# Performance work log

Measured on AMD Instinct MI355X. Metric: run time of the kernel, lower is better.

## Reference

```python
import jax, jax.numpy as jnp
import numpy as np


def setup_inputs() -> dict:
    key = jax.random.key(0)
    ks = jax.random.split(key, 7)
    B, T, I, H = 64, 512, 128, 1024
    s_ih = 1.0 / np.sqrt(H)
    return {
        "x": jax.random.normal(ks[0], (B, T, I), dtype=jnp.float32),
        "W_ih": jax.random.normal(ks[1], (4 * H, I), dtype=jnp.float32) * s_ih,
        "W_hh": jax.random.normal(ks[2], (4 * H, H), dtype=jnp.float32) * s_ih,
        "b_ih": jax.random.normal(ks[3], (4 * H,), dtype=jnp.float32) * s_ih,
        "b_hh": jax.random.normal(ks[4], (4 * H,), dtype=jnp.float32) * s_ih,
        "fc_w": jax.random.normal(ks[5], (I, H), dtype=jnp.float32) * s_ih,
        "fc_b": jax.random.normal(ks[6], (I,), dtype=jnp.float32) * s_ih,
    }


def _lstm_scan(x, W_ih, W_hh, b_ih, b_hh):
    # x: [B, T, I]; returns h sequence [B, T, H]
    B, T, I = x.shape
    H = W_hh.shape[1]
    # precompute input contributions for all timesteps: [T, B, 4H]
    x_proj = jnp.einsum('bti,gi->tbg', x, W_ih) + (b_ih + b_hh)

    def step(carry, xp):
        h, c = carry
        gates = xp + h @ W_hh.T  # [B, 4H]
        i_g, f_g, g_g, o_g = jnp.split(gates, 4, axis=-1)  # PyTorch order i,f,g,o
        i_g = jax.nn.sigmoid(i_g)
        f_g = jax.nn.sigmoid(f_g)
        g_g = jnp.tanh(g_g)
        o_g = jax.nn.sigmoid(o_g)
        c = f_g * c + i_g * g_g
        h = o_g * jnp.tanh(c)
        return (h, c), h

    h0 = jnp.zeros((B, H), dtype=x.dtype)
    c0 = jnp.zeros((B, H), dtype=x.dtype)
    _, hs = jax.lax.scan(step, (h0, c0), x_proj)  # hs: [T, B, H]
    return jnp.transpose(hs, (1, 0, 2))  # [B, T, H]


def reference(x, W_ih, W_hh, b_ih, b_hh, fc_w, fc_b):
    hs = _lstm_scan(x, W_ih, W_hh, b_ih, b_hh)  # [B, T, H]
    return hs @ fc_w.T + fc_b  # [B, T, I]
```

## Files before the change

kernel.cpp:

```cpp
#include <hip/hip_runtime.h>

#define Tn 512
#define Bn 64
#define In 128
#define Hn 1024
#define GBn 16
#define NGn 4
#define NBLKn 32
#define NCOLn 32
#define ROW64 (Hn / 4)

typedef __attribute__((ext_vector_type(8))) short short8;
typedef __attribute__((ext_vector_type(4))) float f32x4;
typedef unsigned long long u64;
typedef unsigned int u32;

__device__ __forceinline__ short f2bf(float f) {
  u32 u = __builtin_bit_cast(u32, f);
  u32 r = u + 0x7FFFu + ((u >> 16) & 1u);
  return (short)(r >> 16);
}
__device__ __forceinline__ float sigm(float x) { return 1.f / (1.f + __expf(-x)); }
__device__ __forceinline__ float tanh_f(float x) {
  float ax = fabsf(x);
  float e = __expf(-2.f * ax);
  float t = (1.f - e) / (1.f + e);
  return x < 0.f ? -t : t;
}
__device__ __forceinline__ short8 cvt8(const float* p) {
  float4 a0 = *(const float4*)p;
  float4 a1 = *(const float4*)(p + 4);
  short8 w;
  w[0] = f2bf(a0.x); w[1] = f2bf(a0.y); w[2] = f2bf(a0.z); w[3] = f2bf(a0.w);
  w[4] = f2bf(a1.x); w[5] = f2bf(a1.y); w[6] = f2bf(a1.z); w[7] = f2bf(a1.w);
  return w;
}

__global__ void __launch_bounds__(256) cvt_kernel(const float* __restrict__ x,
                                                  unsigned short* __restrict__ xb) {
  size_t idx = ((size_t)blockIdx.x * 256 + threadIdx.x) * 8;
  *(short8*)(xb + idx) = cvt8(x + idx);
}

__global__ void __launch_bounds__(512, 2) lstm_kernel(
    const unsigned short* __restrict__ xb, const float* __restrict__ W_ih,
    const float* __restrict__ W_hh, const float* __restrict__ b_ih,
    const float* __restrict__ b_hh, unsigned short* __restrict__ hsb,
    u64* __restrict__ pp) {
  const int bid = blockIdx.x;
  const int grp = bid >> 5;
  const int hc = bid & 31;
  const int tid = threadIdx.x;
  const int wid = tid >> 6;
  const int lane = tid & 63;
  const int rowsel = lane & 15;
  const int k8 = (lane >> 4) * 8;
  const int gate = wid >> 1;
  const int ct = wid & 1;

  __shared__ unsigned short h_lds[GBn * Hn];
  __shared__ float gates_s[4][16][34];
  __shared__ float bias_s[4][NCOLn];

  if (tid < 128) {
    int gg = tid >> 5, cc = tid & 31;
    int idx = gg * Hn + hc * NCOLn + cc;
    bias_s[gg][cc] = b_ih[idx] + b_hh[idx];
  }

  const int wrow = gate * Hn + hc * NCOLn + ct * 16 + rowsel;
  short8 whh[32];
#pragma unroll
  for (int kt = 0; kt < 32; ++kt)
    whh[kt] = cvt8(W_hh + (size_t)wrow * Hn + kt * 32 + k8);
  short8 wih[4];
#pragma unroll
  for (int kt = 0; kt < 4; ++kt)
    wih[kt] = cvt8(W_ih + (size_t)wrow * In + kt * 32 + k8);
  __syncthreads();

  u64* ppg = pp + (size_t)grp * 2 * (GBn * ROW64);
  const unsigned short* xrow = xb + (size_t)(grp * GBn + rowsel) * (Tn * In);

  const int prow = tid >> 5;
  const int pcol = tid & 31;
  float c_reg = 0.f;

  const int rswz = (rowsel & 7) << 4;
  const int rbase = rowsel * 2048 + k8 * 2;

#pragma clang loop unroll(disable)
  for (int t = 0; t < Tn; ++t) {
    f32x4 acc[4];
#pragma unroll
    for (int q = 0; q < 4; ++q) acc[q] = (f32x4){0.f, 0.f, 0.f, 0.f};

    {
      const unsigned short* xp = xrow + (size_t)t * In + k8;
#pragma unroll
      for (int kt = 0; kt < 4; ++kt) {
        short8 a = *(const short8*)(xp + kt * 32);
        acc[kt] = __builtin_amdgcn_mfma_f32_16x16x32_bf16(a, wih[kt], acc[kt],
                                                          0, 0, 0);
      }
    }

    if (t > 0) {
      const u32 want = (u32)((t - 1) % 255) + 1;
      const u64* src64 = ppg + ((t - 1) & 1) * (GBn * ROW64);
      u64 v[8];
      while (true) {
        bool okv = true;
#pragma unroll
        for (int j = 0; j < 8; ++j) {
          const u64* pl =
              src64 + (2 * wid + (j >> 2)) * ROW64 + (j & 3) * 64 + lane;
          v[j] = __hip_atomic_load(pl, __ATOMIC_RELAXED,
                                   __HIP_MEMORY_SCOPE_AGENT);
        }
#pragma unroll
        for (int j = 0; j < 8; ++j)
          okv = okv && ((u32)(v[j] >> 56) == want);
        if (__all(okv)) break;
        __builtin_amdgcn_s_sleep(1);
      }
#pragma unroll
      for (int j = 0; j < 8; ++j) {
        u32 lo = (u32)v[j], hi = (u32)(v[j] >> 32);
        float f0 = (float)(((int)(lo << 20)) >> 20) * 4.8828125e-4f;
        float f1 = (float)(((int)(lo << 8)) >> 20) * 4.8828125e-4f;
        float f2 = (float)(((int)(hi << 20)) >> 20) * 4.8828125e-4f;
        float f3 = (float)(((int)(hi << 8)) >> 20) * 4.8828125e-4f;
        u32 w01, w23;
        asm("v_cvt_pk_bf16_f32 %0, %1, %2" : "=v"(w01) : "v"(f0), "v"(f1));
        asm("v_cvt_pk_bf16_f32 %0, %1, %2" : "=v"(w23) : "v"(f2), "v"(f3));
        int row = 2 * wid + (j >> 2);
        int byteoff = (row * 2048 + ((j & 3) * 64 + lane) * 8) ^
                      ((row & 7) << 4);
        *(u64*)((char*)h_lds + byteoff) = ((u64)w23 << 32) | (u64)w01;
      }
      __syncthreads();

#pragma unroll
      for (int kt = 0; kt < 32; ++kt) {
        short8 a = *(const short8*)((char*)h_lds + ((rbase + kt * 64) ^ rswz));
        acc[kt & 3] = __builtin_amdgcn_mfma_f32_16x16x32_bf16(a, whh[kt],
                                                              acc[kt & 3], 0, 0, 0);
      }
    }

    f32x4 asum = (acc[0] + acc[1]) + (acc[2] + acc[3]);
#pragma unroll
    for (int r = 0; r < 4; ++r)
      gates_s[gate][(lane >> 4) * 4 + r][ct * 16 + (lane & 15)] = asum[r];
    __syncthreads();

    float iv = gates_s[0][prow][pcol] + bias_s[0][pcol];
    float fv = gates_s[1][prow][pcol] + bias_s[1][pcol];
    float gv = gates_s[2][prow][pcol] + bias_s[2][pcol];
    float ov = gates_s[3][prow][pcol] + bias_s[3][pcol];
    float ig = sigm(iv), fg = sigm(fv), og = sigm(ov), gt = tanh_f(gv);
    c_reg = fg * c_reg + ig * gt;
    float hval = og * tanh_f(c_reg);

    int q12 = (int)rintf(hval * 2048.f);
    q12 = q12 > 2047 ? 2047 : (q12 < -2048 ? -2048 : q12);
    u32 me = (u32)(q12 & 0xFFF) << (12 * (pcol & 1));
    u32 m2 = me | __shfl_xor(me, 1);
    u32 mo = __shfl_xor(m2, 2);
    u32 tag = (u32)(t % 255) + 1;
    if ((pcol & 3) == 0) {
      u64 wv = ((u64)(mo | (tag << 24)) << 32) | (u64)m2;
      __hip_atomic_store(
          ppg + (t & 1) * (GBn * ROW64) + prow * ROW64 + (hc * NCOLn + pcol) / 4,
          wv, __ATOMIC_RELAXED, __HIP_MEMORY_SCOPE_AGENT);
    }
    u32 hb = (u32)(unsigned short)f2bf(hval);
    u32 other = __shfl_xor(hb, 1);
    if (!(tid & 1)) {
      size_t hsidx =
          ((size_t)t * Bn + grp * GBn + prow) * Hn + hc * NCOLn + pcol;
      *(u32*)(hsb + hsidx) = hb | (other << 16);
    }
  }
}

__global__ void __launch_bounds__(256) fc_mfma_kernel(
    const unsigned short* __restrict__ hsb, const unsigned short* __restrict__ fwb,
    const float* __restrict__ fcb, float* __restrict__ out) {
  const int wid = threadIdx.x >> 6;
  const int lane = threadIdx.x & 63;
  const int rowsel = lane & 15;
  const int k8 = (lane >> 4) * 8;
  const int r0 = blockIdx.x * 16;
  const int i0 = wid * 32;
  f32x4 acc0 = {0.f, 0.f, 0.f, 0.f}, acc1 = {0.f, 0.f, 0.f, 0.f};
  const unsigned short* hrow = hsb + (size_t)(r0 + rowsel) * Hn + k8;
  const unsigned short* w0 = fwb + (size_t)(i0 + rowsel) * Hn + k8;
  const unsigned short* w1 = w0 + 16 * Hn;
#pragma unroll 8
  for (int kt = 0; kt < 32; ++kt) {
    short8 a = *(const short8*)(hrow + kt * 32);
    short8 b0 = *(const short8*)(w0 + kt * 32);
    short8 b1 = *(const short8*)(w1 + kt * 32);
    acc0 = __builtin_amdgcn_mfma_f32_16x16x32_bf16(a, b0, acc0, 0, 0, 0);
    acc1 = __builtin_amdgcn_mfma_f32_16x16x32_bf16(a, b1, acc1, 0, 0, 0);
  }
  const int n = lane & 15;
  float bias0 = fcb[i0 + n], bias1 = fcb[i0 + 16 + n];
#pragma unroll
  for (int r = 0; r < 4; ++r) {
    int row = r0 + (lane >> 4) * 4 + r;
    float* op = out + ((size_t)(row & 63) * Tn + (row >> 6)) * In;
    op[i0 + n] = acc0[r] + bias0;
    op[i0 + 16 + n] = acc1[r] + bias1;
  }
}

extern "C" void kernel_launch(void* const* d_in, const int* in_sizes, int n_in,
                              void* d_out, int out_size, void* d_ws,
                              size_t ws_size, hipStream_t stream) {
  const float* x    = (const float*)d_in[0];
  const float* W_ih = (const float*)d_in[1];
  const float* W_hh = (const float*)d_in[2];
  const float* b_ih = (const float*)d_in[3];
  const float* b_hh = (const float*)d_in[4];
  const float* fc_w = (const float*)d_in[5];
  const float* fc_b = (const float*)d_in[6];
  float* out = (float*)d_out;

  const size_t hs_b = (size_t)Tn * Bn * Hn * 2;
  const size_t x_b  = (size_t)Bn * Tn * In * 2;
  const size_t fw_b = (size_t)In * Hn * 2;
  const size_t pp_b = (size_t)NGn * 2 * GBn * ROW64 * 8;

  char* wsc = (char*)d_ws;
  unsigned short* hsb = (unsigned short*)wsc;
  unsigned short* xb  = (unsigned short*)(wsc + hs_b);
  unsigned short* fwb = (unsigned short*)(wsc + hs_b + x_b);
  u64* pp = (u64*)(wsc + hs_b + x_b + fw_b);

  (void)hipMemsetAsync(pp, 0, pp_b, stream);
  hipLaunchKernelGGL(cvt_kernel, dim3((Bn * Tn * In) / (256 * 8)), dim3(256),
                     0, stream, x, xb);
  hipLaunchKernelGGL(cvt_kernel, dim3((In * Hn) / (256 * 8)), dim3(256), 0,
                     stream, fc_w, fwb);
  hipLaunchKernelGGL(lstm_kernel, dim3(NGn * NBLKn), dim3(512), 0, stream, xb,
                     W_ih, W_hh, b_ih, b_hh, hsb, pp);
  hipLaunchKernelGGL(fc_mfma_kernel, dim3((Tn * Bn) / 16), dim3(256), 0,
                     stream, hsb, fwb, fc_b, out);
}
```

Baseline: 1.943 ms.

## Split LSTM hidden columns across 256 blocks and prefetch next-step inputs

Changes the persistent LSTM decomposition from 128 blocks of 512 threads (32 hidden columns each) to 256 blocks of 256 threads (16 columns each). Each wave now handles one gate, so per-block recurrent compute halves while more CUs take part in each timestep. Each wave also polls twice as many flag-tagged words to fill the shared h copy. It additionally prefetches the next timestep's bf16 x inputs into registers to hide load latency. The trade-off is more blocks in the grid-wide spin synchronization and more gather work per block, and the grid must now be co-resident with one block per CU.

```diff
diff --git a/kernel.cpp b/kernel.cpp
--- a/kernel.cpp
+++ b/kernel.cpp
@@ -6,8 +6,8 @@
 #define Hn 1024
 #define GBn 16
 #define NGn 4
-#define NBLKn 32
-#define NCOLn 32
+#define NBLKn 64
+#define NCOLn 16
 #define ROW64 (Hn / 4)
 
 typedef __attribute__((ext_vector_type(8))) short short8;
@@ -42,33 +42,31 @@
   *(short8*)(xb + idx) = cvt8(x + idx);
 }
 
-__global__ void __launch_bounds__(512, 2) lstm_kernel(
+__global__ void __launch_bounds__(256, 1) lstm_kernel(
     const unsigned short* __restrict__ xb, const float* __restrict__ W_ih,
     const float* __restrict__ W_hh, const float* __restrict__ b_ih,
     const float* __restrict__ b_hh, unsigned short* __restrict__ hsb,
     u64* __restrict__ pp) {
   const int bid = blockIdx.x;
-  const int grp = bid >> 5;
-  const int hc = bid & 31;
+  const int grp = bid >> 6;
+  const int hc = bid & 63;
   const int tid = threadIdx.x;
   const int wid = tid >> 6;
   const int lane = tid & 63;
   const int rowsel = lane & 15;
   const int k8 = (lane >> 4) * 8;
-  const int gate = wid >> 1;
-  const int ct = wid & 1;
 
   __shared__ unsigned short h_lds[GBn * Hn];
-  __shared__ float gates_s[4][16][34];
-  __shared__ float bias_s[4][NCOLn];
-
-  if (tid < 128) {
-    int gg = tid >> 5, cc = tid & 31;
+  __shared__ float gates_s[4][16][17];
+  __shared__ float bias_s[4][16];
+
+  if (tid < 64) {
+    int gg = tid >> 4, cc = tid & 15;
     int idx = gg * Hn + hc * NCOLn + cc;
     bias_s[gg][cc] = b_ih[idx] + b_hh[idx];
   }
 
-  const int wrow = gate * Hn + hc * NCOLn + ct * 16 + rowsel;
+  const int wrow = wid * Hn + hc * NCOLn + rowsel;
   short8 whh[32];
 #pragma unroll
   for (int kt = 0; kt < 32; ++kt)
@@ -82,12 +80,17 @@
   u64* ppg = pp + (size_t)grp * 2 * (GBn * ROW64);
   const unsigned short* xrow = xb + (size_t)(grp * GBn + rowsel) * (Tn * In);
 
-  const int prow = tid >> 5;
-  const int pcol = tid & 31;
+  const int prow = tid >> 4;
+  const int pcol = tid & 15;
   float c_reg = 0.f;
 
   const int rswz = (rowsel & 7) << 4;
   const int rbase = rowsel * 2048 + k8 * 2;
+
+  short8 xa[4], xn[4];
+#pragma unroll
+  for (int kt = 0; kt < 4; ++kt)
+    xa[kt] = *(const short8*)(xrow + k8 + kt * 32);
 
 #pragma clang loop unroll(disable)
   for (int t = 0; t < Tn; ++t) {
@@ -95,37 +98,37 @@
 #pragma unroll
     for (int q = 0; q < 4; ++q) acc[q] = (f32x4){0.f, 0.f, 0.f, 0.f};
 
+#pragma unroll
+    for (int kt = 0; kt < 4; ++kt)
+      acc[kt] = __builtin_amdgcn_mfma_f32_16x16x32_bf16(xa[kt], wih[kt],
+                                                        acc[kt], 0, 0, 0);
     {
-      const unsigned short* xp = xrow + (size_t)t * In + k8;
-#pragma unroll
-      for (int kt = 0; kt < 4; ++kt) {
-        short8 a = *(const short8*)(xp + kt * 32);
-        acc[kt] = __builtin_amdgcn_mfma_f32_16x16x32_bf16(a, wih[kt], acc[kt],
-                                                          0, 0, 0);
-      }
+      int tn = (t + 1 < Tn) ? t + 1 : t;
+      const unsigned short* xp = xrow + (size_t)tn * In + k8;
+#pragma unroll
+      for (int kt = 0; kt < 4; ++kt) xn[kt] = *(const short8*)(xp + kt * 32);
     }
 
     if (t > 0) {
       const u32 want = (u32)((t - 1) % 255) + 1;
       const u64* src64 = ppg + ((t - 1) & 1) * (GBn * ROW64);
-      u64 v[8];
+      u64 v[16];
       while (true) {
         bool okv = true;
 #pragma unroll
-        for (int j = 0; j < 8; ++j) {
+        for (int j = 0; j < 16; ++j) {
           const u64* pl =
-              src64 + (2 * wid + (j >> 2)) * ROW64 + (j & 3) * 64 + lane;
+              src64 + (4 * wid + (j >> 2)) * ROW64 + (j & 3) * 64 + lane;
           v[j] = __hip_atomic_load(pl, __ATOMIC_RELAXED,
                                    __HIP_MEMORY_SCOPE_AGENT);
         }
 #pragma unroll
-        for (int j = 0; j < 8; ++j)
-          okv = okv && ((u32)(v[j] >> 56) == want);
+        for (int j = 0; j < 16; ++j) okv = okv && ((u32)(v[j] >> 56) == want);
         if (__all(okv)) break;
         __builtin_amdgcn_s_sleep(1);
       }
 #pragma unroll
-      for (int j = 0; j < 8; ++j) {
+      for (int j = 0; j < 16; ++j) {
         u32 lo = (u32)v[j], hi = (u32)(v[j] >> 32);
         float f0 = (float)(((int)(lo << 20)) >> 20) * 4.8828125e-4f;
         float f1 = (float)(((int)(lo << 8)) >> 20) * 4.8828125e-4f;
@@ -134,9 +137,9 @@
         u32 w01, w23;
         asm("v_cvt_pk_bf16_f32 %0, %1, %2" : "=v"(w01) : "v"(f0), "v"(f1));
         asm("v_cvt_pk_bf16_f32 %0, %1, %2" : "=v"(w23) : "v"(f2), "v"(f3));
-        int row = 2 * wid + (j >> 2);
-        int byteoff = (row * 2048 + ((j & 3) * 64 + lane) * 8) ^
-                      ((row & 7) << 4);
+        int row = 4 * wid + (j >> 2);
+        int c4 = (j & 3) * 64 + lane;
+        int byteoff = (row * 2048 + c4 * 8) ^ ((row & 7) << 4);
         *(u64*)((char*)h_lds + byteoff) = ((u64)w23 << 32) | (u64)w01;
       }
       __syncthreads();
@@ -152,7 +155,7 @@
     f32x4 asum = (acc[0] + acc[1]) + (acc[2] + acc[3]);
 #pragma unroll
     for (int r = 0; r < 4; ++r)
-      gates_s[gate][(lane >> 4) * 4 + r][ct * 16 + (lane & 15)] = asum[r];
+      gates_s[wid][(lane >> 4) * 4 + r][lane & 15] = asum[r];
     __syncthreads();
 
     float iv = gates_s[0][prow][pcol] + bias_s[0][pcol];
@@ -172,7 +175,7 @@
     if ((pcol & 3) == 0) {
       u64 wv = ((u64)(mo | (tag << 24)) << 32) | (u64)m2;
       __hip_atomic_store(
-          ppg + (t & 1) * (GBn * ROW64) + prow * ROW64 + (hc * NCOLn + pcol) / 4,
+          ppg + (t & 1) * (GBn * ROW64) + prow * ROW64 + ((hc * NCOLn + pcol) >> 2),
           wv, __ATOMIC_RELAXED, __HIP_MEMORY_SCOPE_AGENT);
     }
     u32 hb = (u32)(unsigned short)f2bf(hval);
@@ -182,6 +185,9 @@
           ((size_t)t * Bn + grp * GBn + prow) * Hn + hc * NCOLn + pcol;
       *(u32*)(hsb + hsidx) = hb | (other << 16);
     }
+
+#pragma unroll
+    for (int kt = 0; kt < 4; ++kt) xa[kt] = xn[kt];
   }
 }
 
@@ -245,7 +251,7 @@
                      0, stream, x, xb);
   hipLaunchKernelGGL(cvt_kernel, dim3((In * Hn) / (256 * 8)), dim3(256), 0,
                      stream, fc_w, fwb);
-  hipLaunchKernelGGL(lstm_kernel, dim3(NGn * NBLKn), dim3(512), 0, stream, xb,
+  hipLaunchKernelGGL(lstm_kernel, dim3(NGn * NBLKn), dim3(256), 0, stream, xb,
                      W_ih, W_hh, b_ih, b_hh, hsb, pp);
   hipLaunchKernelGGL(fc_mfma_kernel, dim3((Tn * Bn) / 16), dim3(256), 0,
                      stream, hsb, fwb, fc_b, out);
```

New measurement: 1.603 ms. -17.5%, faster.
